# Performance work log

Hardware: AMD Instinct MI355X
Metric: run time of the kernel (lower is better)

## Reference

```python
import jax, jax.numpy as jnp
import numpy as np

D_MODEL = 1024
N_HEADS = 16
D_FF = 4096
EPS = 1e-5


def _linear_init(key, fan_in, fan_out):
    # torch nn.Linear default: U(-1/sqrt(fan_in), 1/sqrt(fan_in))
    k1, k2 = jax.random.split(key)
    bound = 1.0 / np.sqrt(fan_in)
    W = jax.random.uniform(k1, (fan_in, fan_out), minval=-bound, maxval=bound, dtype=jnp.float32)
    b = jax.random.uniform(k2, (fan_out,), minval=-bound, maxval=bound, dtype=jnp.float32)
    return W, b


def setup_inputs() -> dict:
    key = jax.random.key(0)
    ks = jax.random.split(key, 8)
    x = jax.random.normal(ks[0], (4, 2048, D_MODEL), dtype=jnp.float32)
    Wq, bq = _linear_init(ks[1], D_MODEL, D_MODEL)
    Wk, bk = _linear_init(ks[2], D_MODEL, D_MODEL)
    Wv, bv = _linear_init(ks[3], D_MODEL, D_MODEL)
    Wo, bo = _linear_init(ks[4], D_MODEL, D_MODEL)
    W1, b1 = _linear_init(ks[5], D_MODEL, D_FF)
    W2, b2 = _linear_init(ks[6], D_FF, D_MODEL)
    g1 = jnp.ones((D_MODEL,), jnp.float32); be1 = jnp.zeros((D_MODEL,), jnp.float32)
    g2 = jnp.ones((D_MODEL,), jnp.float32); be2 = jnp.zeros((D_MODEL,), jnp.float32)
    return {"x": x, "Wq": Wq, "bq": bq, "Wk": Wk, "bk": bk, "Wv": Wv, "bv": bv,
            "Wo": Wo, "bo": bo, "g1": g1, "be1": be1, "W1": W1, "b1": b1,
            "W2": W2, "b2": b2, "g2": g2, "be2": be2}


def _layernorm(x, g, b):
    mu = jnp.mean(x, axis=-1, keepdims=True)
    var = jnp.mean(jnp.square(x - mu), axis=-1, keepdims=True)
    return (x - mu) * jax.lax.rsqrt(var + EPS) * g + b


def reference(x, Wq, bq, Wk, bk, Wv, bv, Wo, bo, g1, be1, W1, b1, W2, b2, g2, be2):
    B, T, D = x.shape
    H, dk = N_HEADS, D // N_HEADS
    # projections -> [B, H, T, dk]
    def split_heads(y):
        return y.reshape(B, T, H, dk).transpose(0, 2, 1, 3)
    Q = split_heads(x @ Wq + bq)
    K = split_heads(x @ Wk + bk)
    V = split_heads(x @ Wv + bv)
    scores = jnp.einsum('bhtd,bhsd->bhts', Q, K) / jnp.sqrt(jnp.float32(dk))
    weights = jax.nn.softmax(scores, axis=-1)  # no causal mask in original
    ctx = jnp.einsum('bhts,bhsd->bhtd', weights, V)
    ctx = ctx.transpose(0, 2, 1, 3).reshape(B, T, D)
    attn_out = ctx @ Wo + bo
    x = _layernorm(x + attn_out, g1, be1)
    ff = jax.nn.relu(x @ W1 + b1) @ W2 + b2
    x = _layernorm(x + ff, g2, be2)
    return x
```

## Files before the change

### kernel.cpp

```cpp
#include <hip/hip_runtime.h>
#include <hip/hip_bf16.h>
#include <stdint.h>

typedef __attribute__((ext_vector_type(8))) short short8;
typedef __attribute__((ext_vector_type(4))) float f32x4;
typedef __attribute__((ext_vector_type(16))) float f32x16;

#define SEQ 2048
#define DMODEL 1024
#define NH 16
#define DKH 64

__device__ __forceinline__ uint16_t f2b(float f) {
  uint32_t u = __float_as_uint(f);
  uint32_t r = (u + 0x7fff + ((u >> 16) & 1)) >> 16;
  return (uint16_t)r;
}
__device__ __forceinline__ float b2f(uint16_t u) {
  return __uint_as_float(((uint32_t)u) << 16);
}

__device__ __forceinline__ void gload16(const uint16_t* g, uint16_t* l) {
  __builtin_amdgcn_global_load_lds((const __attribute__((address_space(1))) void*)g,
                                   (__attribute__((address_space(3))) void*)l, 16, 0, 0);
}

__global__ __launch_bounds__(256) void k_prep(
    const float* __restrict__ Wq, const float* __restrict__ Wk, const float* __restrict__ Wv,
    const float* __restrict__ Wo, const float* __restrict__ W1, const float* __restrict__ W2,
    const float* __restrict__ x, uint16_t* __restrict__ wt_qkv, uint16_t* __restrict__ wt_o,
    uint16_t* __restrict__ wt_1, uint16_t* __restrict__ wt_2, uint16_t* __restrict__ xb) {
  const int id = blockIdx.x;
  if (id >= 12288) {
    int i = (id - 12288) * 256 + threadIdx.x;
    float4 v = reinterpret_cast<const float4*>(x)[i];
    uint16_t o[4] = {f2b(v.x), f2b(v.y), f2b(v.z), f2b(v.w)};
    reinterpret_cast<uint2*>(xb)[i] = *reinterpret_cast<uint2*>(o);
    return;
  }
  __shared__ float tile[32][33];
  const float* W;
  uint16_t* Wt;
  int K, N, bx, by;
  if (id < 4096) {
    int wsel = id >> 10, r = id & 1023;
    K = 1024; N = 1024; bx = r & 31; by = r >> 5;
    W = wsel == 0 ? Wq : (wsel == 1 ? Wk : (wsel == 2 ? Wv : Wo));
    Wt = wsel == 3 ? wt_o : wt_qkv + wsel * 1024 * 1024;
  } else if (id < 8192) {
    int r = id - 4096;
    K = 1024; N = 4096; bx = r & 127; by = r >> 7;
    W = W1; Wt = wt_1;
  } else {
    int r = id - 8192;
    K = 4096; N = 1024; bx = r & 31; by = r >> 5;
    W = W2; Wt = wt_2;
  }
  const int n0 = bx * 32, k0 = by * 32;
  const int tx = threadIdx.x & 31, ty = threadIdx.x >> 5;
#pragma unroll
  for (int i = 0; i < 32; i += 8)
    tile[ty + i][tx] = W[(size_t)(k0 + ty + i) * N + n0 + tx];
  __syncthreads();
#pragma unroll
  for (int i = 0; i < 32; i += 8)
    Wt[(size_t)(n0 + ty + i) * K + k0 + tx] = f2b(tile[tx][ty + i]);
}

#define MODE_QKV 0
#define MODE_RAWB 1
#define MODE_RELU 2

template <int BN, int MODE>
__global__ __launch_bounds__(512, 2) void k_gemm2(
    const uint16_t* __restrict__ A, const uint16_t* __restrict__ Bt, int M, int N, int K,
    int nx, const float* __restrict__ bias0, const float* __restrict__ bias1,
    const float* __restrict__ bias2, uint16_t* __restrict__ ob0, uint16_t* __restrict__ ob1,
    uint16_t* __restrict__ ob2, float* __restrict__ of) {
  constexpr int ASZ = 256 * 64;
  constexpr int BSZ = BN * 64;
  __shared__ __align__(16) uint16_t lds[2 * (ASZ + BSZ)];
  uint16_t* const Abase = lds;
  uint16_t* const Bbase = lds + 2 * ASZ;
  constexpr int WN = (BN == 256) ? 4 : 2;
  constexpr int MREP = (BN == 256) ? 8 : 4;
  constexpr int NPH = (BN == 256) ? 4 : 2;
  const int o = blockIdx.x;
  const int chunk = gridDim.x >> 3;
  const int wg = (o & 7) * chunk + (o >> 3);
  const int brow = (wg / nx) << 8;
  const int bcol = (wg % nx) * BN;
  const int t = threadIdx.x;
  const int wid = t >> 6, l = t & 63, g = l >> 4, lr = l & 15;
  const int wr = wid / WN, wc = wid % WN;
  const int wrow = wr * (MREP * 16);
  const int wcol = wc * 64;

  const int srow = t >> 3;
  const int ss0 = (t & 7) ^ (srow & 7);
  const int ss1 = (t & 7) ^ ((srow + 64) & 7);

  auto stage_half = [&](const uint16_t* gsrc, int grow0, int kk, uint16_t* ldst) {
    gload16(gsrc + (size_t)(grow0 + srow) * K + kk + ss0 * 8, ldst + t * 8);
    gload16(gsrc + (size_t)(grow0 + srow + 64) * K + kk + ss1 * 8, ldst + 4096 + t * 8);
  };
  auto rdfrag = [&](const uint16_t* buf, int ar, int kk) -> short8 {
    int slot = ((kk << 2) + g) ^ (ar & 7);
    return *reinterpret_cast<const short8*>(buf + ar * 64 + slot * 8);
  };

  f32x4 acc[MREP][4] = {};
  const int nt = K >> 6;

  stage_half(A, brow, 0, Abase);
  stage_half(A, brow + 128, 0, Abase + 8192);
  stage_half(Bt, bcol, 0, Bbase);
  if (BN == 256) stage_half(Bt, bcol + 128, 0, Bbase + 8192);
  __syncthreads();

  for (int kt = 0; kt < nt; ++kt) {
    const int cur = kt & 1;
    const uint16_t* Ac = Abase + cur * ASZ;
    const uint16_t* Bc = Bbase + cur * BSZ;
    uint16_t* An = Abase + (cur ^ 1) * ASZ;
    uint16_t* Bn = Bbase + (cur ^ 1) * BSZ;
    const bool pf = (kt + 1 < nt);
    const int knx = (kt + 1) << 6;
#pragma unroll
    for (int q = 0; q < NPH; ++q) {
      const int mq = (BN == 256) ? (q >> 1) : 0;
      const int nq = (BN == 256) ? (q & 1) : q;
      short8 af[4][2], bf[2][2];
#pragma unroll
      for (int j = 0; j < 4; ++j)
#pragma unroll
        for (int kk = 0; kk < 2; ++kk)
          af[j][kk] = rdfrag(Ac, wrow + (mq * 4 + j) * 16 + lr, kk);
#pragma unroll
      for (int j = 0; j < 2; ++j)
#pragma unroll
        for (int kk = 0; kk < 2; ++kk)
          bf[j][kk] = rdfrag(Bc, wcol + (nq * 2 + j) * 16 + lr, kk);
      if (pf && q == 0) {
        stage_half(A, brow, knx, An);
        stage_half(A, brow + 128, knx, An + 8192);
        stage_half(Bt, bcol, knx, Bn);
        if (BN == 256) stage_half(Bt, bcol + 128, knx, Bn + 8192);
      }
      __builtin_amdgcn_s_barrier();
      __builtin_amdgcn_s_setprio(1);
#pragma unroll
      for (int j = 0; j < 4; ++j)
#pragma unroll
        for (int j2 = 0; j2 < 2; ++j2)
#pragma unroll
          for (int kk = 0; kk < 2; ++kk)
            acc[mq * 4 + j][nq * 2 + j2] = __builtin_amdgcn_mfma_f32_16x16x32_bf16(
                af[j][kk], bf[j2][kk], acc[mq * 4 + j][nq * 2 + j2], 0, 0, 0);
      __builtin_amdgcn_s_setprio(0);
      if (q == NPH - 1) {
        asm volatile("s_waitcnt vmcnt(0)" ::: "memory");
        __builtin_amdgcn_s_barrier();
        __builtin_amdgcn_sched_barrier(0);
      } else {
        __builtin_amdgcn_s_barrier();
      }
    }
  }

  if (MODE == MODE_QKV && bcol >= 2048) {
    const int dbase = bcol - 2048;
#pragma unroll
    for (int m = 0; m < MREP; ++m) {
#pragma unroll
      for (int n = 0; n < 4; ++n) {
        const int cl = wcol + n * 16 + lr;
        const float bb = bias2[dbase + cl];
        uint16_t pk[4];
#pragma unroll
        for (int qi = 0; qi < 4; ++qi) pk[qi] = f2b(acc[m][n][qi] + bb);
        const int r0 = wrow + m * 16 + g * 4;
        *reinterpret_cast<uint2*>(&lds[cl * 264 + r0]) = *reinterpret_cast<uint2*>(pk);
      }
    }
    __syncthreads();
    const int bV = brow >> 11;
    const int tt0 = brow & 2047;
#pragma unroll
    for (int j = 0; j < 8; ++j) {
      int ch = j * 512 + t;
      int dl = ch >> 5, sc = ch & 31;
      short8 vv = *reinterpret_cast<const short8*>(&lds[dl * 264 + sc * 8]);
      int hd = dbase + dl;
      int h2 = hd >> 6, d = hd & 63;
      *reinterpret_cast<short8*>(ob2 + ((size_t)(bV * NH + h2)) * SEQ * DKH + (size_t)d * SEQ +
                                 tt0 + sc * 8) = vv;
    }
    return;
  }
#pragma unroll
  for (int m = 0; m < MREP; ++m) {
#pragma unroll
    for (int n = 0; n < 4; ++n) {
#pragma unroll
      for (int qi = 0; qi < 4; ++qi) {
        int r = brow + wrow + m * 16 + g * 4 + qi;
        int c = bcol + wcol + n * 16 + lr;
        float v = acc[m][n][qi];
        if (MODE == MODE_QKV) {
          int which = c >> 10;
          int hd = c & 1023;
          const float* bp = which == 0 ? bias0 : bias1;
          v += bp[hd];
          if (which == 0) v *= 0.1803368801f;
          uint16_t* dst = which == 0 ? ob0 : ob1;
          int b = r >> 11, tt = r & 2047;
          int h = hd >> 6, d = hd & 63;
          dst[((size_t)((b * NH + h) * SEQ + tt)) * DKH + d] = f2b(v);
        } else if (MODE == MODE_RELU) {
          v += bias0[c];
          v = fmaxf(v, 0.0f);
          ob0[(size_t)r * N + c] = f2b(v);
        } else {
          ob0[(size_t)r * N + c] = f2b(v);
        }
      }
    }
  }
}

__global__ __launch_bounds__(256) void k_attn(const uint16_t* __restrict__ Qb,
                                              const uint16_t* __restrict__ Kb,
                                              const uint16_t* __restrict__ Vtg,
                                              uint16_t* __restrict__ ctx) {
  __shared__ __align__(16) uint16_t Ks[2][64 * 64];
  __shared__ __align__(16) uint16_t Vs[2][64 * 64];
  __shared__ float l_arr[4][32];
  const int o = blockIdx.x;
  const int wg = (o & 7) * 128 + (o >> 3);
  const int qt = wg & 15;
  const int bh = wg >> 4;
  const int b = bh >> 4, h = bh & 15;
  const uint16_t* Qp = Qb + (size_t)bh * SEQ * DKH;
  const uint16_t* Kp = Kb + (size_t)bh * SEQ * DKH;
  const uint16_t* Vp = Vtg + (size_t)bh * SEQ * DKH;
  const int t = threadIdx.x, w = t >> 6, l = t & 63;
  const int lo5 = l & 31, hh = l >> 5;
  const int qbase = qt * 128 + w * 32;

  short8 qf[4];
#pragma unroll
  for (int kc = 0; kc < 4; ++kc)
    qf[kc] = *reinterpret_cast<const short8*>(Qp + (size_t)(qbase + lo5) * DKH + kc * 16 + hh * 8);

  f32x16 oacc[2] = {};
  float lsum = 0.f;

  const int swz = ((l & 7) ^ ((l >> 3) & 7)) << 3;
  const int ci0 = w * 2, ci1 = w * 2 + 1;
  const int r0 = ci0 * 8 + (l >> 3), r1 = ci1 * 8 + (l >> 3);
  uint16_t* ldsK0 = &Ks[0][0] + ci0 * 512 + l * 8;
  uint16_t* ldsK1 = &Ks[0][0] + ci1 * 512 + l * 8;
  uint16_t* ldsV0 = &Vs[0][0] + ci0 * 512 + l * 8;
  uint16_t* ldsV1 = &Vs[0][0] + ci1 * 512 + l * 8;
  const uint16_t* gK0 = Kp + (size_t)r0 * DKH + swz;
  const uint16_t* gK1 = Kp + (size_t)r1 * DKH + swz;
  const uint16_t* gV0 = Vp + (size_t)r0 * SEQ + swz;
  const uint16_t* gV1 = Vp + (size_t)r1 * SEQ + swz;

  gload16(gK0, ldsK0);
  gload16(gK1, ldsK1);
  gload16(gV0, ldsV0);
  gload16(gV1, ldsV1);
  __syncthreads();

  for (int tile = 0; tile < 32; ++tile) {
    const int cur = tile & 1;
    if (tile < 31) {
      const int nxt = (cur ^ 1) * 4096;
      const size_t s0n = (size_t)(tile + 1) * 64;
      gload16(gK0 + s0n * DKH, ldsK0 + nxt);
      gload16(gK1 + s0n * DKH, ldsK1 + nxt);
      gload16(gV0 + s0n, ldsV0 + nxt);
      gload16(gV1 + s0n, ldsV1 + nxt);
    }
    const char* Kbuf = reinterpret_cast<const char*>(&Ks[cur][0]);
    const char* Vbuf = reinterpret_cast<const char*>(&Vs[cur][0]);

#pragma unroll
    for (int sblk = 0; sblk < 2; ++sblk) {
      short8 kf[4];
      const int krow = sblk * 32 + lo5;
      const int kxor = (krow & 7) << 4;
#pragma unroll
      for (int kc = 0; kc < 4; ++kc) {
        int cb = (kc * 32 + hh * 16) ^ kxor;
        kf[kc] = *reinterpret_cast<const short8*>(Kbuf + krow * 128 + cb);
      }
      short8 vf[2][2];
#pragma unroll
      for (int scl = 0; scl < 2; ++scl)
#pragma unroll
        for (int dblk = 0; dblk < 2; ++dblk) {
          int vrow = dblk * 32 + lo5;
          int cb = (sblk * 64 + scl * 32 + hh * 16) ^ ((vrow & 7) << 4);
          vf[scl][dblk] = *reinterpret_cast<const short8*>(Vbuf + vrow * 128 + cb);
        }

      f32x16 sa = {};
      __builtin_amdgcn_s_setprio(1);
#pragma unroll
      for (int kc = 0; kc < 4; ++kc)
        sa = __builtin_amdgcn_mfma_f32_32x32x16_bf16(kf[kc], qf[kc], sa, 0, 0, 0);
      __builtin_amdgcn_s_setprio(0);

      float p[16];
      float ls = 0.f;
#pragma unroll
      for (int r = 0; r < 16; ++r) {
        p[r] = __builtin_amdgcn_exp2f(sa[r]);
        ls += p[r];
      }
      lsum += ls;

      uint32_t clo[4], chi[4];
#pragma unroll
      for (int m = 0; m < 4; ++m) {
        asm("v_cvt_pk_bf16_f32 %0, %1, %2" : "=v"(clo[m]) : "v"(p[4 * m]), "v"(p[4 * m + 1]));
        asm("v_cvt_pk_bf16_f32 %0, %1, %2" : "=v"(chi[m]) : "v"(p[4 * m + 2]), "v"(p[4 * m + 3]));
      }

#pragma unroll
      for (int scl = 0; scl < 2; ++scl) {
        uint32_t a0 = clo[2 * scl], b0 = clo[2 * scl + 1];
        uint32_t a1 = chi[2 * scl], b1 = chi[2 * scl + 1];
        asm("v_permlane32_swap_b32 %0, %1" : "+v"(a0), "+v"(b0));
        asm("v_permlane32_swap_b32 %0, %1" : "+v"(a1), "+v"(b1));
        union {
          uint32_t u[4];
          short8 s;
        } pu;
        pu.u[0] = a0;
        pu.u[1] = a1;
        pu.u[2] = b0;
        pu.u[3] = b1;
        __builtin_amdgcn_s_setprio(1);
#pragma unroll
        for (int dblk = 0; dblk < 2; ++dblk)
          oacc[dblk] = __builtin_amdgcn_mfma_f32_32x32x16_bf16(pu.s, vf[scl][dblk], oacc[dblk], 0, 0, 0);
        __builtin_amdgcn_s_setprio(0);
      }
    }
    __syncthreads();
  }

  {
    float full = lsum + __shfl_xor(lsum, 32, 64);
    if (l < 32) l_arr[w][lo5] = full;
  }
#pragma unroll
  for (int r = 0; r < 16; ++r) {
    int q = (r & 3) + 8 * (r >> 2) + 4 * hh;
    float li = 1.0f / l_arr[w][q];
    int rowg = b * SEQ + qbase + q;
#pragma unroll
    for (int dblk = 0; dblk < 2; ++dblk) {
      int colg = h * DKH + dblk * 32 + lo5;
      ctx[(size_t)rowg * DMODEL + colg] = f2b(oacc[dblk][r] * li);
    }
  }
}

template <bool WRITE_B, bool INBF, bool RESBF>
__global__ __launch_bounds__(256) void k_ln(const void* __restrict__ in,
                                            const float* __restrict__ bias,
                                            const void* __restrict__ res,
                                            const float* __restrict__ gam,
                                            const float* __restrict__ bet,
                                            float* __restrict__ outf,
                                            uint16_t* __restrict__ outb) {
  const int row = blockIdx.x;
  const int t = threadIdx.x, lane = t & 63, w = t >> 6;
  float4 v;
  if (INBF) {
    uint2 iu = reinterpret_cast<const uint2*>((const uint16_t*)in + (size_t)row * DMODEL)[t];
    const uint16_t* ip = reinterpret_cast<const uint16_t*>(&iu);
    v.x = b2f(ip[0]); v.y = b2f(ip[1]); v.z = b2f(ip[2]); v.w = b2f(ip[3]);
  } else {
    v = reinterpret_cast<const float4*>((const float*)in + (size_t)row * DMODEL)[t];
  }
  float4 bb0 = reinterpret_cast<const float4*>(bias)[t];
  float4 rr;
  if (RESBF) {
    uint2 ru = reinterpret_cast<const uint2*>((const uint16_t*)res + (size_t)row * DMODEL)[t];
    const uint16_t* rp = reinterpret_cast<const uint16_t*>(&ru);
    rr.x = b2f(rp[0]); rr.y = b2f(rp[1]); rr.z = b2f(rp[2]); rr.w = b2f(rp[3]);
  } else {
    rr = reinterpret_cast<const float4*>((const float*)res + (size_t)row * DMODEL)[t];
  }
  v.x += bb0.x + rr.x;
  v.y += bb0.y + rr.y;
  v.z += bb0.z + rr.z;
  v.w += bb0.w + rr.w;
  float s = v.x + v.y + v.z + v.w;
  float s2 = v.x * v.x + v.y * v.y + v.z * v.z + v.w * v.w;
#pragma unroll
  for (int off = 1; off < 64; off <<= 1) {
    s += __shfl_xor(s, off, 64);
    s2 += __shfl_xor(s2, off, 64);
  }
  __shared__ float rs[4], rq[4];
  if (lane == 0) {
    rs[w] = s;
    rq[w] = s2;
  }
  __syncthreads();
  float ts = rs[0] + rs[1] + rs[2] + rs[3];
  float tq = rq[0] + rq[1] + rq[2] + rq[3];
  const float inv = 1.0f / DMODEL;
  float mu = ts * inv;
  float var = tq * inv - mu * mu;
  float rstd = rsqrtf(var + 1e-5f);
  float4 gg = reinterpret_cast<const float4*>(gam)[t];
  float4 bb = reinterpret_cast<const float4*>(bet)[t];
  float4 y;
  y.x = (v.x - mu) * rstd * gg.x + bb.x;
  y.y = (v.y - mu) * rstd * gg.y + bb.y;
  y.z = (v.z - mu) * rstd * gg.z + bb.z;
  y.w = (v.w - mu) * rstd * gg.w + bb.w;
  if (WRITE_B) {
    uint16_t oo[4] = {f2b(y.x), f2b(y.y), f2b(y.z), f2b(y.w)};
    reinterpret_cast<uint2*>(outb)[(size_t)row * 256 + t] = *reinterpret_cast<uint2*>(oo);
  } else {
    reinterpret_cast<float4*>(outf)[(size_t)row * 256 + t] = y;
  }
}

extern "C" void kernel_launch(void* const* d_in, const int* in_sizes, int n_in, void* d_out,
                              int out_size, void* d_ws, size_t ws_size, hipStream_t stream) {
  const float* x = (const float*)d_in[0];
  const float* Wq = (const float*)d_in[1];
  const float* bq = (const float*)d_in[2];
  const float* Wk = (const float*)d_in[3];
  const float* bk = (const float*)d_in[4];
  const float* Wv = (const float*)d_in[5];
  const float* bv = (const float*)d_in[6];
  const float* Wo = (const float*)d_in[7];
  const float* bo = (const float*)d_in[8];
  const float* g1 = (const float*)d_in[9];
  const float* be1 = (const float*)d_in[10];
  const float* W1 = (const float*)d_in[11];
  const float* b1 = (const float*)d_in[12];
  const float* W2 = (const float*)d_in[13];
  const float* b2 = (const float*)d_in[14];
  const float* g2 = (const float*)d_in[15];
  const float* be2 = (const float*)d_in[16];

  char* ws = (char*)d_ws;
  size_t off = 0;
  auto alloc = [&](size_t bytes) {
    char* p = ws + off;
    off += (bytes + 255) & ~(size_t)255;
    return p;
  };
  uint16_t* wt_qkv = (uint16_t*)alloc(3072ull * 1024 * 2);
  uint16_t* wt_o = (uint16_t*)alloc(1024ull * 1024 * 2);
  uint16_t* wt_1 = (uint16_t*)alloc(4096ull * 1024 * 2);
  uint16_t* wt_2 = (uint16_t*)alloc(1024ull * 4096 * 2);
  uint16_t* xb = (uint16_t*)alloc(8192ull * 1024 * 2);
  uint16_t* ctx = (uint16_t*)alloc(8192ull * 1024 * 2);
  uint16_t* bfout = (uint16_t*)alloc(8192ull * 1024 * 2);
  uint16_t* vt = (uint16_t*)alloc(8192ull * 1024 * 2);
  char* big = alloc(16777216ull + 67108864ull);
  uint16_t* Qbuf = (uint16_t*)big;
  uint16_t* Kbuf = (uint16_t*)(big + 16777216ull);
  uint16_t* x1b = (uint16_t*)big;
  uint16_t* hbuf = (uint16_t*)(big + 16777216ull);
  (void)ws_size;

  k_prep<<<20480, 256, 0, stream>>>(Wq, Wk, Wv, Wo, W1, W2, x, wt_qkv, wt_o, wt_1, wt_2, xb);
  k_gemm2<128, MODE_QKV><<<768, 512, 0, stream>>>(
      xb, wt_qkv, 8192, 3072, 1024, 24, bq, bk, bv, Qbuf, Kbuf, vt, nullptr);
  k_attn<<<1024, 256, 0, stream>>>(Qbuf, Kbuf, vt, ctx);
  k_gemm2<128, MODE_RAWB><<<256, 512, 0, stream>>>(
      ctx, wt_o, 8192, 1024, 1024, 8, nullptr, nullptr, nullptr, bfout, nullptr, nullptr, nullptr);
  k_ln<true, true, true><<<8192, 256, 0, stream>>>(bfout, bo, xb, g1, be1, nullptr, x1b);
  k_gemm2<256, MODE_RELU><<<512, 512, 0, stream>>>(
      x1b, wt_1, 8192, 4096, 1024, 16, b1, nullptr, nullptr, hbuf, nullptr, nullptr, nullptr);
  k_gemm2<128, MODE_RAWB><<<256, 512, 0, stream>>>(
      hbuf, wt_2, 8192, 1024, 4096, 8, nullptr, nullptr, nullptr, bfout, nullptr, nullptr, nullptr);
  k_ln<false, true, true><<<8192, 256, 0, stream>>>(bfout, b2, x1b, g2, be2, (float*)d_out, nullptr);
}
```

Measured before the change: 389.3 us.

## Split GEMM prefetch into per-phase half-tile loads with fine-grained vmcnt waits

Reworks the double-buffered GEMM main loop so each phase issues one half-tile global-to-LDS prefetch instead of issuing all prefetches at phase zero. Each phase waits only on the loads it needs, using partial vmcnt counts. The warp-to-tile mapping is changed so that each phase reads only the A/B halves that have already arrived. This spreads memory traffic across the k-step and removes the end-of-step full drain, at the cost of intricate counter bookkeeping that breaks if the load ordering changes.

```diff
diff --git a/kernel.cpp b/kernel.cpp
--- a/kernel.cpp
+++ b/kernel.cpp
@@ -85,6 +85,8 @@
   constexpr int WN = (BN == 256) ? 4 : 2;
   constexpr int MREP = (BN == 256) ? 8 : 4;
   constexpr int NPH = (BN == 256) ? 4 : 2;
+  constexpr int MJ = (BN == 256) ? 4 : 2;
+  constexpr int NJ = (BN == 256) ? 2 : 4;
   const int o = blockIdx.x;
   const int chunk = gridDim.x >> 3;
   const int wg = (o & 7) * chunk + (o >> 3);
@@ -93,8 +95,14 @@
   const int t = threadIdx.x;
   const int wid = t >> 6, l = t & 63, g = l >> 4, lr = l & 15;
   const int wr = wid / WN, wc = wid % WN;
-  const int wrow = wr * (MREP * 16);
-  const int wcol = wc * 64;
+
+  auto rowb = [&](int m) {
+    return (BN == 256) ? ((m >> 2) * 128 + wr * 64 + (m & 3) * 16)
+                       : ((m >> 1) * 128 + wr * 32 + (m & 1) * 16);
+  };
+  auto colb = [&](int n) {
+    return (BN == 256) ? ((n >> 1) * 128 + wc * 32 + (n & 1) * 16) : (wc * 64 + n * 16);
+  };
 
   const int srow = t >> 3;
   const int ss0 = (t & 7) ^ (srow & 7);
@@ -112,11 +120,16 @@
   f32x4 acc[MREP][4] = {};
   const int nt = K >> 6;
 
-  stage_half(A, brow, 0, Abase);
-  stage_half(A, brow + 128, 0, Abase + 8192);
-  stage_half(Bt, bcol, 0, Bbase);
-  if (BN == 256) stage_half(Bt, bcol + 128, 0, Bbase + 8192);
-  __syncthreads();
+  if (BN == 256) {
+    stage_half(A, brow, 0, Abase);
+    stage_half(Bt, bcol, 0, Bbase);
+    stage_half(Bt, bcol + 128, 0, Bbase + 8192);
+    stage_half(A, brow + 128, 0, Abase + 8192);
+  } else {
+    stage_half(A, brow, 0, Abase);
+    stage_half(Bt, bcol, 0, Bbase);
+    stage_half(A, brow + 128, 0, Abase + 8192);
+  }
 
   for (int kt = 0; kt < nt; ++kt) {
     const int cur = kt & 1;
@@ -128,58 +141,80 @@
     const int knx = (kt + 1) << 6;
 #pragma unroll
     for (int q = 0; q < NPH; ++q) {
-      const int mq = (BN == 256) ? (q >> 1) : 0;
-      const int nq = (BN == 256) ? (q & 1) : q;
-      short8 af[4][2], bf[2][2];
-#pragma unroll
-      for (int j = 0; j < 4; ++j)
+      if (BN == 256) {
+        if (q == 0) {
+          asm volatile("s_waitcnt vmcnt(4)" ::: "memory");
+        } else if (q == 1) {
+          if (pf) asm volatile("s_waitcnt vmcnt(4)" ::: "memory");
+          else asm volatile("s_waitcnt vmcnt(2)" ::: "memory");
+        } else if (q == 2) {
+          if (pf) asm volatile("s_waitcnt vmcnt(4)" ::: "memory");
+          else asm volatile("s_waitcnt vmcnt(0)" ::: "memory");
+        }
+      } else {
+        if (q == 0) {
+          asm volatile("s_waitcnt vmcnt(2)" ::: "memory");
+        } else {
+          if (pf) asm volatile("s_waitcnt vmcnt(4)" ::: "memory");
+          else asm volatile("s_waitcnt vmcnt(0)" ::: "memory");
+        }
+      }
+      __builtin_amdgcn_s_barrier();
+      __builtin_amdgcn_sched_barrier(0);
+      if (pf) {
+        if (BN == 256) {
+          if (q == 0) stage_half(A, brow, knx, An);
+          else if (q == 1) stage_half(Bt, bcol, knx, Bn);
+          else if (q == 2) stage_half(Bt, bcol + 128, knx, Bn + 8192);
+          else stage_half(A, brow + 128, knx, An + 8192);
+        } else {
+          if (q == 0) {
+            stage_half(A, brow, knx, An);
+            stage_half(Bt, bcol, knx, Bn);
+          } else {
+            stage_half(A, brow + 128, knx, An + 8192);
+          }
+        }
+      }
+      const int mq = (BN == 256) ? (q >> 1) : q;
+      const int nq = (BN == 256) ? (q & 1) : 0;
+      short8 af[MJ][2], bf[NJ][2];
+#pragma unroll
+      for (int j = 0; j < MJ; ++j)
 #pragma unroll
         for (int kk = 0; kk < 2; ++kk)
-          af[j][kk] = rdfrag(Ac, wrow + (mq * 4 + j) * 16 + lr, kk);
-#pragma unroll
-      for (int j = 0; j < 2; ++j)
+          af[j][kk] = rdfrag(Ac, rowb(mq * MJ + j) + lr, kk);
+#pragma unroll
+      for (int j2 = 0; j2 < NJ; ++j2)
 #pragma unroll
         for (int kk = 0; kk < 2; ++kk)
-          bf[j][kk] = rdfrag(Bc, wcol + (nq * 2 + j) * 16 + lr, kk);
-      if (pf && q == 0) {
-        stage_half(A, brow, knx, An);
-        stage_half(A, brow + 128, knx, An + 8192);
-        stage_half(Bt, bcol, knx, Bn);
-        if (BN == 256) stage_half(Bt, bcol + 128, knx, Bn + 8192);
-      }
-      __builtin_amdgcn_s_barrier();
+          bf[j2][kk] = rdfrag(Bc, colb(nq * NJ + j2) + lr, kk);
       __builtin_amdgcn_s_setprio(1);
 #pragma unroll
-      for (int j = 0; j < 4; ++j)
-#pragma unroll
-        for (int j2 = 0; j2 < 2; ++j2)
+      for (int j = 0; j < MJ; ++j)
+#pragma unroll
+        for (int j2 = 0; j2 < NJ; ++j2)
 #pragma unroll
           for (int kk = 0; kk < 2; ++kk)
-            acc[mq * 4 + j][nq * 2 + j2] = __builtin_amdgcn_mfma_f32_16x16x32_bf16(
-                af[j][kk], bf[j2][kk], acc[mq * 4 + j][nq * 2 + j2], 0, 0, 0);
+            acc[mq * MJ + j][nq * NJ + j2] = __builtin_amdgcn_mfma_f32_16x16x32_bf16(
+                af[j][kk], bf[j2][kk], acc[mq * MJ + j][nq * NJ + j2], 0, 0, 0);
       __builtin_amdgcn_s_setprio(0);
-      if (q == NPH - 1) {
-        asm volatile("s_waitcnt vmcnt(0)" ::: "memory");
-        __builtin_amdgcn_s_barrier();
-        __builtin_amdgcn_sched_barrier(0);
-      } else {
-        __builtin_amdgcn_s_barrier();
-      }
     }
   }
 
   if (MODE == MODE_QKV && bcol >= 2048) {
     const int dbase = bcol - 2048;
+    __syncthreads();
 #pragma unroll
     for (int m = 0; m < MREP; ++m) {
 #pragma unroll
       for (int n = 0; n < 4; ++n) {
-        const int cl = wcol + n * 16 + lr;
+        const int cl = colb(n) + lr;
         const float bb = bias2[dbase + cl];
         uint16_t pk[4];
 #pragma unroll
         for (int qi = 0; qi < 4; ++qi) pk[qi] = f2b(acc[m][n][qi] + bb);
-        const int r0 = wrow + m * 16 + g * 4;
+        const int r0 = rowb(m) + g * 4;
         *reinterpret_cast<uint2*>(&lds[cl * 264 + r0]) = *reinterpret_cast<uint2*>(pk);
       }
     }
@@ -204,8 +239,8 @@
     for (int n = 0; n < 4; ++n) {
 #pragma unroll
       for (int qi = 0; qi < 4; ++qi) {
-        int r = brow + wrow + m * 16 + g * 4 + qi;
-        int c = bcol + wcol + n * 16 + lr;
+        int r = brow + rowb(m) + g * 4 + qi;
+        int c = bcol + colb(n) + lr;
         float v = acc[m][n][qi];
         if (MODE == MODE_QKV) {
           int which = c >> 10;
```

Measured after the change: 383.0 us. No clear change (-1.6%).
